# Kernel tuning notes

Measured on AMD Instinct MI355X. Metric: run time of the kernel, lower is better.

Reference implementation:

```python
import jax, jax.numpy as jnp
import numpy as np

DIM = 8
EPS = 1e-6
TRIL = DIM * (DIM + 1) // 2  # 36


def _build_L(params):
    # params: [N, TRIL] -> lower-triangular L: [N, DIM, DIM] with diag clamped >= 1e-4
    rows, cols = jnp.tril_indices(DIM)
    L = jnp.zeros((params.shape[0], DIM, DIM), params.dtype)
    L = L.at[:, rows, cols].set(params)
    idx = jnp.arange(DIM)
    d = jnp.clip(L[:, idx, idx], 0.0001)
    return L.at[:, idx, idx].set(d)


def _compute_density(L):
    # L: [N, DIM, DIM] -> PSD trace-1 density matrices [N, DIM, DIM]
    I = jnp.eye(DIM, dtype=L.dtype)
    rho = jnp.einsum('nij,nkj->nik', L, L) + EPS * I
    w = jnp.linalg.eigvalsh(rho)                      # [N, DIM]
    corr = jnp.maximum(-w.min(axis=-1), 0.0) + 1e-6   # shift to PSD
    rho = rho + corr[:, None, None] * I
    tr = jnp.trace(rho, axis1=1, axis2=2)
    return rho / (tr[:, None, None] + EPS)


def _matrix_sqrt(x):
    U, S, Vh = jnp.linalg.svd(x, full_matrices=False)
    sqrt_S = jnp.sqrt(S + EPS)
    return (U * sqrt_S[..., None, :]) @ Vh


def _quantum_fidelity(rho, sigma):
    sqrt_rho = _matrix_sqrt(rho)
    product = sqrt_rho @ sigma @ sqrt_rho
    S = jnp.linalg.svd(product, compute_uv=False)
    f = jnp.sum(jnp.sqrt(S + EPS), axis=-1)
    return jnp.clip(f, 0.0, 1.0)


def setup_inputs() -> dict:
    key = jax.random.key(0)
    k1, k2, k3 = jax.random.split(key, 3)
    B, S, V = 16384, 10, 100000
    contexts = jax.random.randint(k1, (B, S), 0, V)
    targets = jax.random.randint(k2, (B,), 0, V)
    # embedding table, init roughly like the torch module (uniform + diag ramp)
    emb_weight = jax.random.uniform(k3, (V, TRIL), jnp.float32, -0.1, 0.1)
    diag_idx = np.array([i * (i + 1) // 2 + i for i in range(DIM)])
    diag_vals = jnp.linspace(0.1, 1.0, DIM, dtype=jnp.float32)
    emb_weight = emb_weight.at[:, diag_idx].set(jnp.broadcast_to(diag_vals, (V, DIM)))
    return {"contexts": contexts, "targets": targets, "emb_weight": emb_weight}


def reference(contexts, targets, emb_weight):
    B, S = contexts.shape
    # context density matrices
    ctx_params = jnp.take(emb_weight, contexts.reshape(-1), axis=0)   # [B*S, TRIL]
    rho_ctx = _compute_density(_build_L(ctx_params)).reshape(B, S, DIM, DIM)
    mask = (contexts != 0).astype(rho_ctx.dtype)[:, :, None, None]
    context_rho = (rho_ctx * mask).sum(axis=1) / mask.sum(axis=1)     # [B, DIM, DIM]
    # target density matrices
    tgt_params = jnp.take(emb_weight, targets, axis=0)                # [B, TRIL]
    rho_tgt = _compute_density(_build_L(tgt_params))                  # [B, DIM, DIM]
    f = _quantum_fidelity(context_rho, rho_tgt)                       # [B]
    return -jnp.log(jnp.clip(f, 1e-8))
```

## Files before the change

kernel.cpp:

```cpp
#include <hip/hip_runtime.h>
#include <math.h>

#define NB   16384
#define SEQ  10
#define DIM  8
#define TRIL 36

__device__ __forceinline__ constexpr int tri(int r, int c) { return r * (r + 1) / 2 + c; }

__device__ __forceinline__ double fast_rsqrt(double x) {
    double r = __builtin_amdgcn_rsq(x);
    r = r * (1.5 - 0.5 * x * r * r);
    r = r * (1.5 - 0.5 * x * r * r);
    return r;
}
__device__ __forceinline__ double fast_rcp(double x) {
    double r = __builtin_amdgcn_rcp(x);
    r = r * (2.0 - x * r);
    r = r * (2.0 - x * r);
    return r;
}
__device__ __forceinline__ double fast_sqrt(double x) { return x * fast_rsqrt(x); }

template <bool ACCUM>
__device__ __forceinline__ void add_density(const float* __restrict__ p, double (&dst)[TRIL]) {
    float Lf[TRIL];
    const float4* p4 = (const float4*)p;
    #pragma unroll
    for (int i = 0; i < 9; ++i) {
        float4 v = p4[i];
        Lf[4*i+0] = v.x; Lf[4*i+1] = v.y; Lf[4*i+2] = v.z; Lf[4*i+3] = v.w;
    }
    #pragma unroll
    for (int d = 0; d < DIM; ++d) Lf[tri(d, d)] = fmaxf(Lf[tri(d, d)], 1.0e-4f);

    double tr = 1.6e-5;
    #pragma unroll
    for (int i = 0; i < TRIL; ++i) { double v = (double)Lf[i]; tr += v * v; }
    double inv = fast_rcp(tr + 1.0e-6);

    #pragma unroll
    for (int i = 0; i < DIM; ++i) {
        #pragma unroll
        for (int j = 0; j <= i; ++j) {
            double sum = (i == j) ? 2.0e-6 : 0.0;
            #pragma unroll
            for (int k = 0; k <= j; ++k) sum += (double)Lf[tri(i, k)] * (double)Lf[tri(j, k)];
            if (ACCUM) dst[tri(i, j)] += sum * inv;
            else       dst[tri(i, j)]  = sum * inv;
        }
    }
}

__device__ __forceinline__ void chol36(double (&M)[TRIL]) {
    #pragma unroll
    for (int j = 0; j < DIM; ++j) {
        double d = M[tri(j, j)];
        #pragma unroll
        for (int k = 0; k < j; ++k) d -= M[tri(j, k)] * M[tri(j, k)];
        d = fmax(d, 1.0e-30);
        double invd = fast_rsqrt(d);
        M[tri(j, j)] = d * invd;
        #pragma unroll
        for (int i = j + 1; i < DIM; ++i) {
            double v = M[tri(i, j)];
            #pragma unroll
            for (int k = 0; k < j; ++k) v -= M[tri(i, k)] * M[tri(j, k)];
            M[tri(i, j)] = v * invd;
        }
    }
}

__global__ void __launch_bounds__(64)
qcbow_kernel(const int* __restrict__ contexts,
             const int* __restrict__ targets,
             const float* __restrict__ emb,
             float* __restrict__ out)
{
    const int tid = blockIdx.x * 64 + threadIdx.x;
    const int b = tid >> 2;
    const int g = threadIdx.x & 3;

    double A[TRIL];
    #pragma unroll
    for (int i = 0; i < TRIL; ++i) A[i] = 0.0;
    double cnt = 0.0;
    for (int s = g; s < SEQ; s += 4) {
        int tok = contexts[b * SEQ + s];
        if (tok != 0) {
            add_density<true>(emb + (size_t)tok * TRIL, A);
            cnt += 1.0;
        }
    }

    double W[TRIL];
    add_density<false>(emb + (size_t)targets[b] * TRIL, W);

    #pragma unroll
    for (int i = 0; i < TRIL; ++i) A[i] += __shfl_xor(A[i], 1, 4);
    cnt += __shfl_xor(cnt, 1, 4);
    #pragma unroll
    for (int i = 0; i < TRIL; ++i) A[i] += __shfl_xor(A[i], 2, 4);
    cnt += __shfl_xor(cnt, 2, 4);

    chol36(W);

    double invc = fast_rcp(cnt);
    #pragma unroll
    for (int i = 0; i < TRIL; ++i) A[i] *= invc;
    #pragma unroll
    for (int d = 0; d < DIM; ++d) A[tri(d, d)] += 1.0e-6;
    chol36(A);

    double wa[DIM], wb[DIM];
#define PICKW(JA, JB)                                                              \
    {                                                                              \
        _Pragma("unroll")                                                          \
        for (int k = 0; k < DIM; ++k) wa[k] = (k >= (JA)) ? W[tri(k, (JA))] : 0.0; \
        _Pragma("unroll")                                                          \
        for (int k = 0; k < DIM; ++k) wb[k] = (k >= (JB)) ? W[tri(k, (JB))] : 0.0; \
    }
    switch (g) {
        case 0: PICKW(0, 1); break;
        case 1: PICKW(2, 3); break;
        case 2: PICKW(4, 5); break;
        default: PICKW(6, 7); break;
    }
#undef PICKW

    double a[DIM], bc[DIM];
    #pragma unroll
    for (int i = 0; i < DIM; ++i) {
        double sa = 0.0, sb = 0.0;
        #pragma unroll
        for (int k = i; k < DIM; ++k) {
            double lk = A[tri(k, i)];
            sa += lk * wa[k];
            sb += lk * wb[k];
        }
        a[i] = sa; bc[i] = sb;
    }

    for (int sweep = 0; sweep < 10; ++sweep) {
        double maxz2 = 0.0;
        #pragma unroll
        for (int r = 0; r < 7; ++r) {
            double x = 0.0, y = 0.0, z = 0.0;
            #pragma unroll
            for (int k = 0; k < DIM; ++k) {
                x += a[k] * a[k];
                y += bc[k] * bc[k];
                z += a[k] * bc[k];
            }
            double z2 = z * z;
            maxz2 = fmax(maxz2, z2);
            if (z2 > 1.0e-20) {
                float tauf = (float)(y - x) * (0.5f * __builtin_amdgcn_rcpf((float)z));
                float tf = __builtin_amdgcn_rcpf(fabsf(tauf) + sqrtf(1.0f + tauf * tauf));
                tf = (tauf >= 0.0f) ? tf : -tf;
                double t = (double)tf;
                double x2 = 1.0 + t * t;
                double c = (double)__builtin_amdgcn_rsqf((float)x2);
                c = c * (1.5 - 0.5 * x2 * c * c);
                double s = t * c;
                #pragma unroll
                for (int k = 0; k < DIM; ++k) {
                    double na = c * a[k] - s * bc[k];
                    double nb = s * a[k] + c * bc[k];
                    a[k] = na; bc[k] = nb;
                }
            }
            #pragma unroll
            for (int k = 0; k < DIM; ++k) {
                double olda = a[k];
                double sa = (g == 0) ? bc[k] : a[k];
                double ta = __shfl(sa, (g + 3) & 3, 4);
                double tb = __shfl(bc[k], (g + 1) & 3, 4);
                a[k]  = (g == 0) ? olda : ta;
                bc[k] = (g == 3) ? olda : tb;
            }
        }
        if (sweep >= 2 && __all(maxz2 < 1.0e-18)) break;
    }

    double x = 0.0, y = 0.0;
    #pragma unroll
    for (int k = 0; k < DIM; ++k) { x += a[k] * a[k]; y += bc[k] * bc[k]; }
    double fp = fast_sqrt(x + 1.0e-6) + fast_sqrt(y + 1.0e-6);
    fp += __shfl_xor(fp, 1, 4);
    fp += __shfl_xor(fp, 2, 4);
    if (g == 0) {
        double f = fmin(fp, 1.0);
        f = fmax(f, 1.0e-8);
        out[b] = (float)(-log(f));
    }
}

extern "C" void kernel_launch(void* const* d_in, const int* in_sizes, int n_in,
                              void* d_out, int out_size, void* d_ws, size_t ws_size,
                              hipStream_t stream) {
    const int*   contexts = (const int*)d_in[0];
    const int*   targets  = (const int*)d_in[1];
    const float* emb      = (const float*)d_in[2];
    float*       out      = (float*)d_out;

    qcbow_kernel<<<dim3(NB * 4 / 64), dim3(64), 0, stream>>>(contexts, targets, emb, out);
}
```

Measured before the change: 94.98 us.

## Run Jacobi SVD sweeps in fp32 and use DPP lane permutes for shuffles

Moves the one-sided Jacobi rotation loop from double to single precision, switches to a relative convergence test and caps sweeps at 8 instead of 10. All quad-level shuffles (the reduction and the rotation of columns between lanes) now use DPP quad_perm moves instead of __shfl, which avoids LDS-based bpermute traffic. FP64 is far slower than FP32 on this GPU, so the Jacobi inner loop should get much cheaper. The cost is possible loss of accuracy in the fidelity when singular values are small.

```diff
diff --git a/kernel.cpp b/kernel.cpp
--- a/kernel.cpp
+++ b/kernel.cpp
@@ -7,6 +7,20 @@
 #define TRIL 36
 
 __device__ __forceinline__ constexpr int tri(int r, int c) { return r * (r + 1) / 2 + c; }
+
+template <int CTRL>
+__device__ __forceinline__ float fperm(float v) {
+    return __int_as_float(__builtin_amdgcn_mov_dpp(__float_as_int(v), CTRL, 0xf, 0xf, true));
+}
+template <int CTRL>
+__device__ __forceinline__ double dperm(double v) {
+    long long u = __double_as_longlong(v);
+    int lo = (int)(u & 0xffffffffLL);
+    int hi = (int)(u >> 32);
+    lo = __builtin_amdgcn_mov_dpp(lo, CTRL, 0xf, 0xf, true);
+    hi = __builtin_amdgcn_mov_dpp(hi, CTRL, 0xf, 0xf, true);
+    return __longlong_as_double(((long long)hi << 32) | (long long)(unsigned)lo);
+}
 
 __device__ __forceinline__ double fast_rsqrt(double x) {
     double r = __builtin_amdgcn_rsq(x);
@@ -84,12 +98,12 @@
     double A[TRIL];
     #pragma unroll
     for (int i = 0; i < TRIL; ++i) A[i] = 0.0;
-    double cnt = 0.0;
+    float cntf = 0.0f;
     for (int s = g; s < SEQ; s += 4) {
         int tok = contexts[b * SEQ + s];
         if (tok != 0) {
             add_density<true>(emb + (size_t)tok * TRIL, A);
-            cnt += 1.0;
+            cntf += 1.0f;
         }
     }
 
@@ -97,15 +111,15 @@
     add_density<false>(emb + (size_t)targets[b] * TRIL, W);
 
     #pragma unroll
-    for (int i = 0; i < TRIL; ++i) A[i] += __shfl_xor(A[i], 1, 4);
-    cnt += __shfl_xor(cnt, 1, 4);
-    #pragma unroll
-    for (int i = 0; i < TRIL; ++i) A[i] += __shfl_xor(A[i], 2, 4);
-    cnt += __shfl_xor(cnt, 2, 4);
+    for (int i = 0; i < TRIL; ++i) A[i] += dperm<0xB1>(A[i]);
+    cntf += fperm<0xB1>(cntf);
+    #pragma unroll
+    for (int i = 0; i < TRIL; ++i) A[i] += dperm<0x4E>(A[i]);
+    cntf += fperm<0x4E>(cntf);
 
     chol36(W);
 
-    double invc = fast_rcp(cnt);
+    double invc = fast_rcp((double)cntf);
     #pragma unroll
     for (int i = 0; i < TRIL; ++i) A[i] *= invc;
     #pragma unroll
@@ -128,7 +142,7 @@
     }
 #undef PICKW
 
-    double a[DIM], bc[DIM];
+    float a[DIM], bb[DIM];
     #pragma unroll
     for (int i = 0; i < DIM; ++i) {
         double sa = 0.0, sb = 0.0;
@@ -138,57 +152,58 @@
             sa += lk * wa[k];
             sb += lk * wb[k];
         }
-        a[i] = sa; bc[i] = sb;
-    }
-
-    for (int sweep = 0; sweep < 10; ++sweep) {
-        double maxz2 = 0.0;
+        a[i] = (float)sa; bb[i] = (float)sb;
+    }
+
+    for (int sweep = 0; sweep < 8; ++sweep) {
+        bool conv = true;
         #pragma unroll
         for (int r = 0; r < 7; ++r) {
-            double x = 0.0, y = 0.0, z = 0.0;
+            float x = 0.0f, y = 0.0f, z = 0.0f;
             #pragma unroll
             for (int k = 0; k < DIM; ++k) {
-                x += a[k] * a[k];
-                y += bc[k] * bc[k];
-                z += a[k] * bc[k];
+                x = fmaf(a[k], a[k], x);
+                y = fmaf(bb[k], bb[k], y);
+                z = fmaf(a[k], bb[k], z);
             }
-            double z2 = z * z;
-            maxz2 = fmax(maxz2, z2);
-            if (z2 > 1.0e-20) {
-                float tauf = (float)(y - x) * (0.5f * __builtin_amdgcn_rcpf((float)z));
-                float tf = __builtin_amdgcn_rcpf(fabsf(tauf) + sqrtf(1.0f + tauf * tauf));
-                tf = (tauf >= 0.0f) ? tf : -tf;
-                double t = (double)tf;
-                double x2 = 1.0 + t * t;
-                double c = (double)__builtin_amdgcn_rsqf((float)x2);
-                c = c * (1.5 - 0.5 * x2 * c * c);
-                double s = t * c;
+            float z2 = z * z;
+            float d  = x - y;
+            if (z2 > 1.0e-12f * x * y && z2 > 1.0e-12f * d * d) conv = false;
+            if (z2 > 1.0e-16f * x * y) {
+                float tau = -d * (0.5f * __builtin_amdgcn_rcpf(z));
+                float t = __builtin_amdgcn_rcpf(fabsf(tau) + sqrtf(fmaf(tau, tau, 1.0f)));
+                t = (tau >= 0.0f) ? t : -t;
+                float c = __builtin_amdgcn_rsqf(fmaf(t, t, 1.0f));
+                float s = t * c;
                 #pragma unroll
                 for (int k = 0; k < DIM; ++k) {
-                    double na = c * a[k] - s * bc[k];
-                    double nb = s * a[k] + c * bc[k];
-                    a[k] = na; bc[k] = nb;
+                    float na = c * a[k] - s * bb[k];
+                    float nb = s * a[k] + c * bb[k];
+                    a[k] = na; bb[k] = nb;
                 }
             }
             #pragma unroll
             for (int k = 0; k < DIM; ++k) {
-                double olda = a[k];
-                double sa = (g == 0) ? bc[k] : a[k];
-                double ta = __shfl(sa, (g + 3) & 3, 4);
-                double tb = __shfl(bc[k], (g + 1) & 3, 4);
+                float olda = a[k];
+                float sa = (g == 0) ? bb[k] : a[k];
+                float ta = fperm<0x93>(sa);
+                float tb = fperm<0x39>(bb[k]);
                 a[k]  = (g == 0) ? olda : ta;
-                bc[k] = (g == 3) ? olda : tb;
+                bb[k] = (g == 3) ? olda : tb;
             }
         }
-        if (sweep >= 2 && __all(maxz2 < 1.0e-18)) break;
-    }
-
-    double x = 0.0, y = 0.0;
-    #pragma unroll
-    for (int k = 0; k < DIM; ++k) { x += a[k] * a[k]; y += bc[k] * bc[k]; }
-    double fp = fast_sqrt(x + 1.0e-6) + fast_sqrt(y + 1.0e-6);
-    fp += __shfl_xor(fp, 1, 4);
-    fp += __shfl_xor(fp, 2, 4);
+        if (sweep >= 2 && __all(conv)) break;
+    }
+
+    double xn = 0.0, yn = 0.0;
+    #pragma unroll
+    for (int k = 0; k < DIM; ++k) {
+        xn += (double)a[k] * (double)a[k];
+        yn += (double)bb[k] * (double)bb[k];
+    }
+    double fp = fast_sqrt(xn + 1.0e-6) + fast_sqrt(yn + 1.0e-6);
+    fp += dperm<0xB1>(fp);
+    fp += dperm<0x4E>(fp);
     if (g == 0) {
         double f = fmin(fp, 1.0);
         f = fmax(f, 1.0e-8);
```

Measured after the change: 85.81 us. 1.11x faster.
